# Kernel optimization log

Hardware: AMD Instinct MI355X
Metric: run time of the kernel (lower is better)

## Reference

```python
import jax, jax.numpy as jnp
import numpy as np
from jax import lax

B, S, H = 2, 2048, 768
FF = 1536
E = 8
TOP_K = 2


def setup_inputs() -> dict:
    key = jax.random.key(0)
    k1, k2, k3, k4 = jax.random.split(key, 4)
    hidden_states = jax.random.normal(k1, (B, S, H), dtype=jnp.float32)
    # torch init: weight.normal_() for experts; nn.Linear default init for gate (approx normal here is fine for a numerics baseline)
    gate_w = jax.random.normal(k2, (E, H), dtype=jnp.float32) * 0.02
    w_fc = jax.random.normal(k3, (E, FF, H), dtype=jnp.float32) * 0.02
    w_proj = jax.random.normal(k4, (E, H, FF), dtype=jnp.float32) * 0.02
    return {"hidden_states": hidden_states, "gate_w": gate_w, "w_fc": w_fc, "w_proj": w_proj}


def reference(hidden_states, gate_w, w_fc, w_proj):
    b, s, h = hidden_states.shape
    x = hidden_states.reshape(-1, h)                      # [T, H]
    # --- top-k gating (logits in float32, as in the torch code) ---
    logits = (x @ gate_w.T).astype(jnp.float32)           # [T, E]
    top_logits, top_idx = lax.top_k(logits, TOP_K)        # [T, K]
    gates = jax.nn.softmax(top_logits, axis=1).astype(x.dtype)  # [T, K]
    # combined per-token/per-expert gate: g[t,e] = sum_k gates[t,k]*[idx[t,k]==e]
    onehot = jax.nn.one_hot(top_idx, E, dtype=x.dtype)    # [T, K, E]
    g = jnp.einsum('tk,tke->te', gates, onehot)           # [T, E]
    # --- experts: gather + per-expert GEMM + gated scatter-add combine ---
    # Equivalent math: tokens with zero gate for expert e contribute nothing,
    # so compute each expert on all tokens and weight by g[:, e].
    out = jnp.zeros_like(x)
    for e in range(E):  # fixed small loop over experts (structurally distinct weights)
        hmid = jax.nn.gelu(x @ w_fc[e].T, approximate=False)   # [T, FF] (torch gelu = erf form)
        out = out + g[:, e:e + 1] * (hmid @ w_proj[e].T)       # [T, H]
    out = out.reshape(b, s, h)
    return out, logits
```

## Files before the change

### kernel.cpp

```cpp
#include <hip/hip_runtime.h>
#include <hip/hip_bf16.h>
#include <math.h>
#include <stdint.h>

#define TOKENS 4096
#define HDIM   768
#define FFDIM  1536
#define NEXP   8
#define GEMM_GRID 1024
#define SLOTS (GEMM_GRID / 8)

typedef __attribute__((ext_vector_type(8))) short bf16x8;
typedef __attribute__((ext_vector_type(4))) float f32x4;

__device__ __forceinline__ unsigned short f2bf(float f) {
    union { float f; uint32_t u; } c; c.f = f;
    uint32_t u = c.u;
    uint32_t r = (u + 0x7FFFu + ((u >> 16) & 1u)) >> 16;
    return (unsigned short)r;
}

__device__ __forceinline__ void gload_lds16(const void* g, void* l) {
    __builtin_amdgcn_global_load_lds(
        (const __attribute__((address_space(1))) void*)g,
        (__attribute__((address_space(3))) void*)l, 16, 0, 0);
}

__global__ void cast_bf16_2(const float* __restrict__ s1, unsigned short* __restrict__ d1,
                            const float* __restrict__ s2, unsigned short* __restrict__ d2,
                            int n4) {
    int stride = gridDim.x * blockDim.x;
    for (int i = blockIdx.x * blockDim.x + threadIdx.x; i < 2 * n4; i += stride) {
        const float4* s = (i < n4) ? (const float4*)s1 : (const float4*)s2;
        ushort4* d = (i < n4) ? (ushort4*)d1 : (ushort4*)d2;
        int j = (i < n4) ? i : i - n4;
        float4 v = s[j];
        ushort4 o;
        o.x = f2bf(v.x); o.y = f2bf(v.y); o.z = f2bf(v.z); o.w = f2bf(v.w);
        d[j] = o;
    }
}

__global__ __launch_bounds__(256) void gating(
    const float* __restrict__ x, const float* __restrict__ gw,
    float* __restrict__ logits,
    int* __restrict__ tok_e, float* __restrict__ tok_g,
    unsigned short* __restrict__ x_bf, float* __restrict__ outp)
{
    float4 zz = make_float4(0.f, 0.f, 0.f, 0.f);
#pragma unroll
    for (int j = 0; j < 3; j++)
        ((float4*)outp)[blockIdx.x * 768 + j * 256 + threadIdx.x] = zz;

    int t = blockIdx.x * 4 + (threadIdx.x >> 6);
    int lane = threadIdx.x & 63;
    const float4* xt = (const float4*)(x + (size_t)t * HDIM);
    const float4* gw4 = (const float4*)gw;
    ushort4* xbt = (ushort4*)(x_bf + (size_t)t * HDIM);
    float acc[NEXP];
#pragma unroll
    for (int e = 0; e < NEXP; e++) acc[e] = 0.f;
#pragma unroll
    for (int it = 0; it < 3; it++) {
        int i = lane + it * 64;
        float4 xv = xt[i];
        ushort4 o;
        o.x = f2bf(xv.x); o.y = f2bf(xv.y); o.z = f2bf(xv.z); o.w = f2bf(xv.w);
        xbt[i] = o;
#pragma unroll
        for (int e = 0; e < NEXP; e++) {
            float4 wv = gw4[e * 192 + i];
            acc[e] += xv.x * wv.x + xv.y * wv.y + xv.z * wv.z + xv.w * wv.w;
        }
    }
#pragma unroll
    for (int e = 0; e < NEXP; e++) {
#pragma unroll
        for (int off = 32; off > 0; off >>= 1)
            acc[e] += __shfl_xor(acc[e], off);
    }
    if (lane == 0) {
        float4 l0 = make_float4(acc[0], acc[1], acc[2], acc[3]);
        float4 l1 = make_float4(acc[4], acc[5], acc[6], acc[7]);
        float4* lp = (float4*)(logits + (size_t)t * NEXP);
        lp[0] = l0; lp[1] = l1;
        int i0 = 0; float v0 = acc[0];
#pragma unroll
        for (int e = 1; e < NEXP; e++) if (acc[e] > v0) { v0 = acc[e]; i0 = e; }
        int i1 = -1; float v1 = -3.4e38f;
#pragma unroll
        for (int e = 0; e < NEXP; e++) if (e != i0 && acc[e] > v1) { v1 = acc[e]; i1 = e; }
        float g0 = 1.f / (1.f + expf(v1 - v0));
        tok_e[t * 2] = i0; tok_e[t * 2 + 1] = i1;
        tok_g[t * 2] = g0; tok_g[t * 2 + 1] = 1.f - g0;
    }
}

__global__ __launch_bounds__(1024) void build_lists(
    const int* __restrict__ tok_e, const float* __restrict__ tok_g,
    int* __restrict__ counts,
    int* __restrict__ entries, float* __restrict__ gates)
{
    __shared__ unsigned long long wlo[16], whi[16];
    int tid = threadIdx.x;
    int lane = tid & 63, wid = tid >> 6;

    int eL[8]; float gL[8];
    int4 ea = ((const int4*)tok_e)[tid * 2];
    int4 eb = ((const int4*)tok_e)[tid * 2 + 1];
    float4 ga = ((const float4*)tok_g)[tid * 2];
    float4 gb = ((const float4*)tok_g)[tid * 2 + 1];
    eL[0] = ea.x; eL[1] = ea.y; eL[2] = ea.z; eL[3] = ea.w;
    eL[4] = eb.x; eL[5] = eb.y; eL[6] = eb.z; eL[7] = eb.w;
    gL[0] = ga.x; gL[1] = ga.y; gL[2] = ga.z; gL[3] = ga.w;
    gL[4] = gb.x; gL[5] = gb.y; gL[6] = gb.z; gL[7] = gb.w;

    unsigned long long clo = 0, chi = 0;
#pragma unroll
    for (int j = 0; j < 8; j++) {
        int e = eL[j];
        unsigned long long one = 1ull << ((e & 3) * 16);
        if (e < 4) clo += one; else chi += one;
    }
    unsigned long long ilo = clo, ihi = chi;
#pragma unroll
    for (int s = 1; s < 64; s <<= 1) {
        unsigned long long t1 = __shfl_up(ilo, s);
        unsigned long long t2 = __shfl_up(ihi, s);
        if (lane >= s) { ilo += t1; ihi += t2; }
    }
    if (lane == 63) { wlo[wid] = ilo; whi[wid] = ihi; }
    __syncthreads();
    if (tid == 0) {
        unsigned long long rl = 0, rh = 0;
#pragma unroll
        for (int i = 0; i < 16; i++) {
            unsigned long long a = wlo[i], b = whi[i];
            wlo[i] = rl; whi[i] = rh;
            rl += a; rh += b;
        }
#pragma unroll
        for (int e = 0; e < 4; e++) {
            counts[e]     = (int)((rl >> (e * 16)) & 0xFFFF);
            counts[e + 4] = (int)((rh >> (e * 16)) & 0xFFFF);
        }
    }
    __syncthreads();
    unsigned long long rlo = wlo[wid] + (ilo - clo);
    unsigned long long rhi = whi[wid] + (ihi - chi);
#pragma unroll
    for (int j = 0; j < 8; j++) {
        int e = eL[j];
        int sh = (e & 3) * 16;
        unsigned long long one = 1ull << sh;
        int slot;
        if (e < 4) { slot = (int)((rlo >> sh) & 0xFFFF); rlo += one; }
        else       { slot = (int)((rhi >> sh) & 0xFFFF); rhi += one; }
        entries[e * TOKENS + slot] = tid * 8 + j;
        gates[e * TOKENS + slot]   = gL[j];
    }
}

template<int KD, int ND, int TN, int NCTP, bool IS_FC>
__global__ __launch_bounds__(256) void moe_gemm(
    const unsigned short* __restrict__ Asrc,
    const unsigned short* __restrict__ Bsrc,
    const int* __restrict__ counts,
    const int* __restrict__ entries,
    const float* __restrict__ gates,
    unsigned short* __restrict__ hmid,
    float* __restrict__ outp)
{
    constexpr int AJ = TN / 32;
    constexpr int CB = TN / 32;
    int bkt  = blockIdx.x & 7;
    int slot = blockIdx.x >> 3;

    int cs[NEXP];
#pragma unroll
    for (int e = 0; e < NEXP; e++) cs[e] = counts[e];
    int n_e = cs[bkt];
    int rts = (n_e + 127) >> 7;
    int nfill = rts * NCTP;
    if (slot >= nfill) return;
    int ebase = 0;
#pragma unroll
    for (int e = 0; e < NEXP; e++) if (e < bkt) ebase += cs[e];
    const int* lst = entries + bkt * TOKENS;

    int tid = threadIdx.x;
    int w = tid >> 6;
    int l = tid & 63;
    int sg = l & 7;
    int lr8 = l >> 3;
    int lo = l & 15;
    int q  = l >> 4;
    int wr = w >> 1, wc = w & 1;

    __shared__ __align__(16) unsigned short sA[128 * 64];
    __shared__ __align__(16) unsigned short sB[TN * 64];

    int aOff[4][2], bOff[AJ][2];
#pragma unroll
    for (int i = 0; i < 4; i++) {
        int m = wr * 64 + i * 16 + lo;
#pragma unroll
        for (int s = 0; s < 2; s++)
            aOff[i][s] = m * 64 + ((s * 4 + q) ^ (m & 7)) * 8;
    }
#pragma unroll
    for (int j = 0; j < AJ; j++) {
        int n = wc * (TN / 2) + j * 16 + lo;
#pragma unroll
        for (int s = 0; s < 2; s++)
            bOff[j][s] = n * 64 + ((s * 4 + q) ^ (n & 7)) * 8;
    }

    for (int p = slot; p < nfill; p += SLOTS) {
        int ct   = p / rts;
        int r    = p - ct * rts;
        int row0 = r << 7;
        int n0 = ct * TN;

        const unsigned short* Ag[4];
        int aLds[4];
#pragma unroll
        for (int c = 0; c < 4; c++) {
            int rr = w * 32 + c * 8 + lr8;
            int gr = row0 + rr;
            int id = gr < n_e ? gr : n_e - 1;
            size_t arow = IS_FC ? (size_t)(lst[id] >> 1) : (size_t)(ebase + id);
            Ag[c] = Asrc + arow * KD + (size_t)((sg ^ (rr & 7)) * 8);
            aLds[c] = (w * 32 + c * 8) * 64;
        }
        const unsigned short* Bg[CB];
        int bLds[CB];
#pragma unroll
        for (int c = 0; c < CB; c++) {
            int rr = w * (TN / 4) + c * 8 + lr8;
            Bg[c] = Bsrc + ((size_t)bkt * ND + n0 + rr) * KD + (size_t)((sg ^ (rr & 7)) * 8);
            bLds[c] = (w * (TN / 4) + c * 8) * 64;
        }

        f32x4 acc[4][AJ];
#pragma unroll
        for (int i = 0; i < 4; i++)
#pragma unroll
            for (int j = 0; j < AJ; j++) acc[i][j] = (f32x4){0.f, 0.f, 0.f, 0.f};

        for (int k0 = 0; k0 < KD; k0 += 64) {
#pragma unroll
            for (int c = 0; c < 4; c++) gload_lds16(Ag[c] + k0, sA + aLds[c]);
#pragma unroll
            for (int c = 0; c < CB; c++) gload_lds16(Bg[c] + k0, sB + bLds[c]);
            __syncthreads();
#pragma unroll
            for (int s = 0; s < 2; s++) {
                bf16x8 a[4], b[AJ];
#pragma unroll
                for (int i = 0; i < 4; i++) a[i] = *(const bf16x8*)(sA + aOff[i][s]);
#pragma unroll
                for (int j = 0; j < AJ; j++) b[j] = *(const bf16x8*)(sB + bOff[j][s]);
#pragma unroll
                for (int i = 0; i < 4; i++)
#pragma unroll
                    for (int j = 0; j < AJ; j++)
                        acc[i][j] = __builtin_amdgcn_mfma_f32_16x16x32_bf16(a[i], b[j], acc[i][j], 0, 0, 0);
            }
            __syncthreads();
        }

#pragma unroll
        for (int i = 0; i < 4; i++) {
            int rowB = row0 + wr * 64 + i * 16 + q * 4;
#pragma unroll
            for (int rr = 0; rr < 4; rr++) {
                int orow = rowB + rr;
                if (orow < n_e) {
                    if (IS_FC) {
                        size_t hrow = (size_t)(ebase + orow);
#pragma unroll
                        for (int j = 0; j < AJ; j++) {
                            float v = acc[i][j][rr];
                            v = 0.5f * v * (1.f + erff(v * 0.70710678118654752f));
                            hmid[hrow * ND + n0 + wc * (TN / 2) + j * 16 + lo] = f2bf(v);
                        }
                    } else {
                        int token = lst[orow] >> 1;
                        float g = gates[bkt * TOKENS + orow];
#pragma unroll
                        for (int j = 0; j < AJ; j++) {
                            atomicAdd(&outp[(size_t)token * ND + n0 + wc * (TN / 2) + j * 16 + lo],
                                      acc[i][j][rr] * g);
                        }
                    }
                }
            }
        }
    }
}

extern "C" void kernel_launch(void* const* d_in, const int* in_sizes, int n_in,
                              void* d_out, int out_size, void* d_ws, size_t ws_size,
                              hipStream_t stream) {
    const float* x     = (const float*)d_in[0];
    const float* gw    = (const float*)d_in[1];
    const float* wfc   = (const float*)d_in[2];
    const float* wproj = (const float*)d_in[3];
    float* outp   = (float*)d_out;
    float* logits = outp + (size_t)TOKENS * HDIM;

    char* ws = (char*)d_ws;
    int*   counts  = (int*)ws;
    size_t off = 256;
    int*   entries = (int*)(ws + off);
    float* gates   = (float*)(ws + off + NEXP * TOKENS * 4);
    off += 2ull * NEXP * TOKENS * 4;
    int*   tok_e   = (int*)(ws + off);   off += (size_t)TOKENS * 2 * 4;
    float* tok_g   = (float*)(ws + off); off += (size_t)TOKENS * 2 * 4;
    unsigned short* x_bf   = (unsigned short*)(ws + off); off += (size_t)TOKENS * HDIM * 2;
    unsigned short* wfc_bf = (unsigned short*)(ws + off); off += (size_t)NEXP * FFDIM * HDIM * 2;
    unsigned short* wpj_bf = (unsigned short*)(ws + off); off += (size_t)NEXP * HDIM * FFDIM * 2;
    unsigned short* hmid   = (unsigned short*)(ws + off);

    cast_bf16_2<<<2048, 256, 0, stream>>>(wfc, wfc_bf, wproj, wpj_bf,
                                          NEXP * FFDIM * HDIM / 4);
    gating<<<TOKENS / 4, 256, 0, stream>>>(x, gw, logits, tok_e, tok_g, x_bf, outp);
    build_lists<<<1, 1024, 0, stream>>>(tok_e, tok_g, counts, entries, gates);
    moe_gemm<HDIM, FFDIM, 128, FFDIM / 128, true ><<<GEMM_GRID, 256, 0, stream>>>(
        x_bf, wfc_bf, counts, entries, gates, hmid, outp);
    moe_gemm<FFDIM, HDIM, 64, HDIM / 64, false><<<GEMM_GRID, 256, 0, stream>>>(
        hmid, wpj_bf, counts, entries, gates, hmid, outp);
}
```

Before: 234.3 us.

## Enlarge MoE GEMM row tile to 256 and double-buffer the projection GEMM

Both expert GEMMs now run 512-thread blocks that cover 256 token rows per tile instead of 128. Each block therefore loads each weight tile once for twice as many rows, cutting weight traffic per row. The projection GEMM also gains a two-stage LDS ping-pong that issues the next k-slice's global-to-LDS loads before computing on the current one, using explicit vmcnt waits, raw barriers and setprio around the MFMA bursts. The cost is half as many tiles per expert, which may leave CUs idle, plus more LDS and register pressure per block.

```diff
diff --git a/kernel.cpp b/kernel.cpp
--- a/kernel.cpp
+++ b/kernel.cpp
@@ -161,8 +161,8 @@
     }
 }
 
-template<int KD, int ND, int TN, int NCTP, bool IS_FC>
-__global__ __launch_bounds__(256) void moe_gemm(
+template<int KD, int ND, int TN, int NCTP, bool IS_FC, bool DBUF>
+__global__ __launch_bounds__(512) void moe_gemm(
     const unsigned short* __restrict__ Asrc,
     const unsigned short* __restrict__ Bsrc,
     const int* __restrict__ counts,
@@ -171,8 +171,10 @@
     unsigned short* __restrict__ hmid,
     float* __restrict__ outp)
 {
+    constexpr int BM = 256;
     constexpr int AJ = TN / 32;
-    constexpr int CB = TN / 32;
+    constexpr int CB = TN / 64;
+    constexpr int NV = 4 + CB;
     int bkt  = blockIdx.x & 7;
     int slot = blockIdx.x >> 3;
 
@@ -180,7 +182,7 @@
 #pragma unroll
     for (int e = 0; e < NEXP; e++) cs[e] = counts[e];
     int n_e = cs[bkt];
-    int rts = (n_e + 127) >> 7;
+    int rts = (n_e + BM - 1) >> 8;
     int nfill = rts * NCTP;
     if (slot >= nfill) return;
     int ebase = 0;
@@ -197,8 +199,12 @@
     int q  = l >> 4;
     int wr = w >> 1, wc = w & 1;
 
-    __shared__ __align__(16) unsigned short sA[128 * 64];
-    __shared__ __align__(16) unsigned short sB[TN * 64];
+    __shared__ __align__(16) unsigned short sA[(DBUF ? 2 : 1) * BM * 64];
+    __shared__ __align__(16) unsigned short sB[(DBUF ? 2 : 1) * TN * 64];
+    unsigned short* sA0 = sA;
+    unsigned short* sA1 = sA + BM * 64;
+    unsigned short* sB0 = sB;
+    unsigned short* sB1 = sB + TN * 64;
 
     int aOff[4][2], bOff[AJ][2];
 #pragma unroll
@@ -219,7 +225,7 @@
     for (int p = slot; p < nfill; p += SLOTS) {
         int ct   = p / rts;
         int r    = p - ct * rts;
-        int row0 = r << 7;
+        int row0 = r << 8;
         int n0 = ct * TN;
 
         const unsigned short* Ag[4];
@@ -237,9 +243,9 @@
         int bLds[CB];
 #pragma unroll
         for (int c = 0; c < CB; c++) {
-            int rr = w * (TN / 4) + c * 8 + lr8;
+            int rr = w * (TN / 8) + c * 8 + lr8;
             Bg[c] = Bsrc + ((size_t)bkt * ND + n0 + rr) * KD + (size_t)((sg ^ (rr & 7)) * 8);
-            bLds[c] = (w * (TN / 4) + c * 8) * 64;
+            bLds[c] = (w * (TN / 8) + c * 8) * 64;
         }
 
         f32x4 acc[4][AJ];
@@ -248,26 +254,61 @@
 #pragma unroll
             for (int j = 0; j < AJ; j++) acc[i][j] = (f32x4){0.f, 0.f, 0.f, 0.f};
 
-        for (int k0 = 0; k0 < KD; k0 += 64) {
-#pragma unroll
-            for (int c = 0; c < 4; c++) gload_lds16(Ag[c] + k0, sA + aLds[c]);
-#pragma unroll
-            for (int c = 0; c < CB; c++) gload_lds16(Bg[c] + k0, sB + bLds[c]);
-            __syncthreads();
+        auto stage = [&](unsigned short* SA, unsigned short* SB, int k0) {
+#pragma unroll
+            for (int c = 0; c < 4; c++) gload_lds16(Ag[c] + k0, SA + aLds[c]);
+#pragma unroll
+            for (int c = 0; c < CB; c++) gload_lds16(Bg[c] + k0, SB + bLds[c]);
+        };
+        auto compute = [&](const unsigned short* SA, const unsigned short* SB) {
 #pragma unroll
             for (int s = 0; s < 2; s++) {
                 bf16x8 a[4], b[AJ];
 #pragma unroll
-                for (int i = 0; i < 4; i++) a[i] = *(const bf16x8*)(sA + aOff[i][s]);
-#pragma unroll
-                for (int j = 0; j < AJ; j++) b[j] = *(const bf16x8*)(sB + bOff[j][s]);
+                for (int i = 0; i < 4; i++) a[i] = *(const bf16x8*)(SA + aOff[i][s]);
+#pragma unroll
+                for (int j = 0; j < AJ; j++) b[j] = *(const bf16x8*)(SB + bOff[j][s]);
 #pragma unroll
                 for (int i = 0; i < 4; i++)
 #pragma unroll
                     for (int j = 0; j < AJ; j++)
                         acc[i][j] = __builtin_amdgcn_mfma_f32_16x16x32_bf16(a[i], b[j], acc[i][j], 0, 0, 0);
             }
-            __syncthreads();
+        };
+
+        if constexpr (!DBUF) {
+            for (int k0 = 0; k0 < KD; k0 += 64) {
+                stage(sA0, sB0, k0);
+                __syncthreads();
+                compute(sA0, sB0);
+                __syncthreads();
+            }
+        } else {
+#define WAITN asm volatile("s_waitcnt vmcnt(%0)" :: "n"(NV) : "memory")
+#define WAIT0 asm volatile("s_waitcnt vmcnt(0)" ::: "memory")
+            stage(sA0, sB0, 0);
+            for (int k0 = 0; k0 < KD; k0 += 128) {
+                stage(sA1, sB1, k0 + 64);
+                WAITN;
+                __builtin_amdgcn_s_barrier();
+                __builtin_amdgcn_s_setprio(1);
+                compute(sA0, sB0);
+                __builtin_amdgcn_s_setprio(0);
+                __builtin_amdgcn_s_barrier();
+                if (k0 + 128 < KD) {
+                    stage(sA0, sB0, k0 + 128);
+                    WAITN;
+                } else {
+                    WAIT0;
+                }
+                __builtin_amdgcn_s_barrier();
+                __builtin_amdgcn_s_setprio(1);
+                compute(sA1, sB1);
+                __builtin_amdgcn_s_setprio(0);
+                __builtin_amdgcn_s_barrier();
+            }
+#undef WAITN
+#undef WAIT0
         }
 
 #pragma unroll
@@ -327,8 +368,8 @@
                                           NEXP * FFDIM * HDIM / 4);
     gating<<<TOKENS / 4, 256, 0, stream>>>(x, gw, logits, tok_e, tok_g, x_bf, outp);
     build_lists<<<1, 1024, 0, stream>>>(tok_e, tok_g, counts, entries, gates);
-    moe_gemm<HDIM, FFDIM, 128, FFDIM / 128, true ><<<GEMM_GRID, 256, 0, stream>>>(
+    moe_gemm<HDIM, FFDIM, 128, FFDIM / 128, true,  false><<<GEMM_GRID, 512, 0, stream>>>(
         x_bf, wfc_bf, counts, entries, gates, hmid, outp);
-    moe_gemm<FFDIM, HDIM, 64, HDIM / 64, false><<<GEMM_GRID, 256, 0, stream>>>(
+    moe_gemm<FFDIM, HDIM, 64,  HDIM / 64,   false, true ><<<GEMM_GRID, 512, 0, stream>>>(
         hmid, wpj_bf, counts, entries, gates, hmid, outp);
 }
```

Result: faster. 223.0 us (-4.8%).
